# Performance work log

Hardware: AMD Instinct MI355X
Metric: run time of the kernel (lower is better)

Reference implementation:

```python
import jax, jax.numpy as jnp
import numpy as np

N_QUBITS = 20
N_LAYERS = 4
BATCH = 16
DIM = 2 ** N_QUBITS


def _apply_ry(state, theta, q, n):
    """Apply RY(theta) = [[cos(t/2), -sin(t/2)], [sin(t/2), cos(t/2)]] on qubit q.
    state: (B, 2**n) complex. Qubit 0 is most significant (qibo convention)."""
    c = jnp.cos(theta / 2).astype(state.dtype)
    s = jnp.sin(theta / 2).astype(state.dtype)
    B = state.shape[0]
    st = state.reshape(B, 2 ** q, 2, 2 ** (n - q - 1))
    a = st[:, :, 0, :]
    b = st[:, :, 1, :]
    new = jnp.stack([c * a - s * b, s * a + c * b], axis=2)
    return new.reshape(B, -1)


def _apply_cnot(state, cq, tq, n):
    """CNOT with control cq < target tq: flip target bit where control bit is 1."""
    B = state.shape[0]
    st = state.reshape(B, 2 ** cq, 2, 2 ** (tq - cq - 1), 2, 2 ** (n - tq - 1))
    ctrl0 = st[:, :, 0]                      # (B, 2^cq, mid, 2, rest)
    ctrl1 = jnp.flip(st[:, :, 1], axis=3)    # swap target |0>/<->|1>
    new = jnp.stack([ctrl0, ctrl1], axis=2)
    return new.reshape(B, -1)


def _run_circuit(state, theta):
    # theta: (N_LAYERS * N_QUBITS,) -> (N_LAYERS, N_QUBITS)
    th = theta.reshape(N_LAYERS, N_QUBITS)
    for l in range(N_LAYERS):
        for q in range(N_QUBITS):
            state = _apply_ry(state, th[l, q], q, N_QUBITS)
        for q in range(N_QUBITS - 1):
            state = _apply_cnot(state, q, q + 1, N_QUBITS)
    return state


def setup_inputs() -> dict:
    key = jax.random.key(0)
    k1, k2 = jax.random.split(key)
    x = jax.random.normal(k1, (BATCH, DIM), dtype=jnp.float32)
    theta = jax.random.normal(k2, (N_LAYERS * N_QUBITS,), dtype=jnp.float32)
    return {"x": x, "theta": theta}


def reference(x, theta):
    state = x.astype(jnp.complex64)  # initial state vector, (B, 2**n)
    state = _run_circuit(state, theta)
    return jnp.abs(state)
```

## Files before the change

### kernel.cpp

```cpp
#include <hip/hip_runtime.h>
#include <math.h>


__global__ void cs_kernel(const float* __restrict__ theta, float2* __restrict__ cs) {
    int i = threadIdx.x;
    if (i < 80) {
        float s, c;
        sincosf(theta[i] * 0.5f, &s, &c);
        cs[i] = make_float2(c, s);
    }
}

#define RYT_(TBL, MASK, Q) { float2 _sc = (TBL)[(Q)]; float _c = _sc.x, _s = _sc.y; \
  _Pragma("unroll") for (int _m = 0; _m < 32; ++_m) if (!(_m & (MASK))) { \
    float _a = v[_m], _b = v[_m | (MASK)]; \
    v[_m] = _c*_a - _s*_b; v[_m | (MASK)] = _s*_a + _c*_b; } }

#define CX_(CM, TM) { _Pragma("unroll") for (int _m = 0; _m < 32; ++_m) \
  if ((_m & (CM)) && !(_m & (TM))) { float _t = v[_m]; v[_m] = v[_m|(TM)]; v[_m|(TM)] = _t; } }

#define CXI_(COND, TM) { if (COND) { _Pragma("unroll") for (int _m = 0; _m < 32; ++_m) \
  if (!(_m & (TM))) { float _t = v[_m]; v[_m] = v[_m|(TM)]; v[_m|(TM)] = _t; } } }

__device__ __forceinline__ int mixR(int n) {
    return ((n >> 5) & 31) ^ ((n >> 10) & 1);
}
__device__ __forceinline__ int mixA(int n) {
    return ((n >> 5) & 31) ^ ((n >> 10) & 1) ^ (((n >> 11) & 1) << 3)
         ^ (((n >> 12) & 1) << 4) ^ (((n >> 13) & 1) << 4);
}
__device__ __forceinline__ int mixF(int n) {
    return ((n >> 5) & 31) ^ (((n >> 10) & 1) << 1) ^ (((n >> 11) & 1) << 2)
         ^ (((n >> 12) & 1) << 3) ^ (((n >> 13) & 1) << 4);
}
__device__ __forceinline__ int mixL(int n) {
    return ((n >> 5) & 31) ^ (((n >> 10) & 1) << 4) ^ (((n >> 11) & 1) << 2)
         ^ (((n >> 12) & 1) << 3) ^ (((n >> 13) & 1) << 4);
}

__global__ __launch_bounds__(512, 4) void pass_R(
    const float4* __restrict__ src, float4* __restrict__ dst,
    const float2* __restrict__ cs)
{
    __shared__ float lds[16384];
    const float2* csl = cs;
    int t = threadIdx.x, blk = blockIdx.x;
    int H = blk & 63, b = blk >> 6;
    int base = (b << 18) + (H << 12);
    float v[32];

#pragma unroll
    for (int i = 0; i < 8; ++i) {
        float4 w = src[base + (i << 8) + (((t >> 6) & 3) << 6) + (((t >> 8) & 1) << 11) + (t & 63)];
        v[i*4+0] = w.x; v[i*4+1] = w.y; v[i*4+2] = w.z; v[i*4+3] = w.w;
    }
    RYT_(csl, 1, 19); RYT_(csl, 2, 18); RYT_(csl, 4, 9); RYT_(csl, 8, 8); RYT_(csl, 16, 7);
    { int w1x = (t & 31) ^ ((t >> 5) & 1);
#pragma unroll
      for (int m = 0; m < 32; ++m) lds[(t << 5) | (m ^ w1x)] = v[m]; }
    __syncthreads();

    { int tp = (t & 31) | (((t >> 5) & 1) << 10) | (((t >> 6) & 7) << 11);
      int mt = mixR(tp);
#pragma unroll
      for (int f = 0; f < 32; ++f) { int fc = f << 5; v[f] = lds[(tp | fc) ^ mt ^ mixR(fc)]; }
      RYT_(csl, 1, 17); RYT_(csl, 2, 16); RYT_(csl, 4, 15); RYT_(csl, 8, 14); RYT_(csl, 16, 13);
#pragma unroll
      for (int f = 0; f < 32; ++f) { int fc = f << 5; lds[(tp | fc) ^ mt ^ mixR(fc)] = v[f]; } }
    __syncthreads();

    { int tp = ((t & 1) << 2) | (((t >> 1) & 1) << 3) | (((t >> 2) & 1) << 4)
             | (((t >> 3) & 1) << 5) | (((t >> 4) & 1) << 1) | (((t >> 5) & 1) << 0)
             | (((t >> 6) & 7) << 6);
      int mt = mixR(tp);
#pragma unroll
      for (int p = 0; p < 32; ++p) { int fc = p << 9; v[p] = lds[(tp | fc) ^ mt ^ mixR(fc)]; }
      RYT_(csl, 2, 12); RYT_(csl, 4, 11); RYT_(csl, 8, 10); RYT_(csl, 16, 6);
      int sb = base + (((t >> 6) & 7) << 6) + (t & 63);
#pragma unroll
      for (int j = 0; j < 8; ++j)
        dst[sb + (j << 9)] = make_float4(v[4*j], v[4*j+1], v[4*j+2], v[4*j+3]); }
}

template <bool FULL>
__global__ __launch_bounds__(512, 4) void pass_A(
    const float4* __restrict__ src, float4* __restrict__ dst,
    const float2* __restrict__ cs, int layer)
{
    __shared__ float lds[16384];
    const float2* csl = cs + layer * 20;
    int t = threadIdx.x, blk = blockIdx.x;
    int G = blk & 63, b = blk >> 6;
    int Gperm = ((G >> 2) & 1) | (((G >> 1) & 1) << 1) | ((G & 1) << 2) | (((G >> 3) & 7) << 3);
    float v[32];

    { int lb = (b << 18) + (((t >> 6) & 7) << 9) + (Gperm << 3) + (t & 7);
      int rg = ((t >> 3) & 7) << 12;
#pragma unroll
      for (int i = 0; i < 8; ++i) {
        float4 w = src[lb + ((i << 3) << 12) + rg];
        v[i*4+0] = w.x; v[i*4+1] = w.y; v[i*4+2] = w.z; v[i*4+3] = w.w;
      } }
    RYT_(csl, 16, 0); RYT_(csl, 8, 1); RYT_(csl, 4, 2);
    if (FULL) { RYT_(csl, 2, 12); RYT_(csl, 1, 13); }
    { int w1x = (t & 31) ^ ((t >> 5) & 1) ^ (((t >> 6) & 1) << 3)
              ^ (((t >> 7) & 1) << 4) ^ (((t >> 8) & 1) << 4);
#pragma unroll
      for (int m = 0; m < 32; ++m) lds[(t << 5) | (m ^ w1x)] = v[m]; }
    __syncthreads();

    { int tp = (t & 3) | (((t >> 2) & 1) << 7) | (((t >> 3) & 1) << 11)
             | (((t >> 4) & 1) << 12) | (((t >> 5) & 1) << 13) | (((t >> 6) & 1) << 5)
             | (((t >> 7) & 1) << 6) | (((t >> 8) & 1) << 8);
      int mt = mixA(tp);
#pragma unroll
      for (int f = 0; f < 32; ++f) {
        int fc = ((f & 1) << 9) | (((f >> 1) & 1) << 10) | (((f >> 2) & 1) << 2)
               | (((f >> 3) & 1) << 3) | (((f >> 4) & 1) << 4);
        v[f] = lds[(tp | fc) ^ mt ^ mixA(fc)]; }
      RYT_(csl, 1, 4); RYT_(csl, 2, 3);
      CX_(16, 8); CX_(8, 4); CX_(4, 2); CX_(2, 1);
#pragma unroll
      for (int f = 0; f < 32; ++f) {
        int fc = ((f & 1) << 9) | (((f >> 1) & 1) << 10) | (((f >> 2) & 1) << 2)
               | (((f >> 3) & 1) << 3) | (((f >> 4) & 1) << 4);
        lds[(tp | fc) ^ mt ^ mixA(fc)] = v[f]; } }
    __syncthreads();

    { int tp = (t & 31) | (((t >> 5) & 1) << 9) | (((t >> 6) & 1) << 10)
             | (((t >> 7) & 1) << 11) | (((t >> 8) & 1) << 12);
      int mt = mixA(tp);
#pragma unroll
      for (int f = 0; f < 32; ++f) {
        int fc = ((f & 1) << 5) | (((f >> 1) & 1) << 6) | (((f >> 2) & 1) << 7)
               | (((f >> 3) & 1) << 13) | (((f >> 4) & 1) << 8);
        v[f] = lds[(tp | fc) ^ mt ^ mixA(fc)]; }
      RYT_(csl, 16, 5);
      if (FULL) { RYT_(csl, 8, 6); RYT_(csl, 4, 7); RYT_(csl, 2, 8); RYT_(csl, 1, 9); }
      CXI_((t >> 5) & 1, 16); CX_(16, 8); CX_(8, 4); CX_(4, 2); CX_(2, 1);
#pragma unroll
      for (int f = 0; f < 32; ++f) {
        int fc = ((f & 1) << 5) | (((f >> 1) & 1) << 6) | (((f >> 2) & 1) << 7)
               | (((f >> 3) & 1) << 13) | (((f >> 4) & 1) << 8);
        lds[(tp | fc) ^ mt ^ mixA(fc)] = v[f]; } }
    __syncthreads();

    { int tp = ((t & 1) << 8) | (((t >> 1) & 1) << 9) | (((t >> 2) & 1) << 10)
             | (((t >> 3) & 1) << 6) | (((t >> 4) & 1) << 7) | (((t >> 5) & 1) << 2)
             | (((t >> 6) & 1) << 5) | (((t >> 7) & 1) << 3) | (((t >> 8) & 1) << 4);
      int mt = mixA(tp);
#pragma unroll
      for (int p = 0; p < 32; ++p) {
        int fc = ((p & 1) << 0) | (((p >> 1) & 1) << 13) | (((p >> 2) & 1) << 1)
               | (((p >> 3) & 1) << 11) | (((p >> 4) & 1) << 12);
        v[p] = lds[(tp | fc) ^ mt ^ mixA(fc)]; }
      if (FULL) { RYT_(csl, 16, 10); RYT_(csl, 8, 11); }
      CXI_((t >> 6) & 1, 16); CX_(16, 8); CX_(8, 4); CX_(4, 1);
      int sb = (b << 18) + (G << 12) + t;
#pragma unroll
      for (int j = 0; j < 8; ++j)
        dst[sb + (j << 9)] = make_float4(v[4*j], v[4*j+1], v[4*j+2], v[4*j+3]); }
}

template <bool LOWRY>
__global__ __launch_bounds__(512, 4) void pass_F(
    const float4* __restrict__ src, float4* __restrict__ dst,
    const float2* __restrict__ cs, int layer)
{
    __shared__ float lds[16384];
    const float2* csl  = cs + layer * 20;
    const float2* csl2 = cs + (layer + 1) * 20;
    int t = threadIdx.x, blk = blockIdx.x;
    int W = blk & 63, b = blk >> 6;
    int Wp = (((W >> 4) & 1) << 3) | (((W >> 5) & 1) << 4) | (((W >> 3) & 1) << 6)
           | ((W & 1) << 9) | (((W >> 1) & 1) << 10) | (((W >> 2) & 1) << 11);
    float v[32];

    { int lb = (((b << 6) | ((t >> 3) & 63)) << 12) + (t & 7) + Wp;
#pragma unroll
      for (int i = 0; i < 8; ++i) {
        float4 w = src[lb + ((i & 1) << 5) + (((i >> 1) & 1) << 7) + (((i >> 2) & 1) << 8)];
        v[i*4+0] = w.x; v[i*4+1] = w.y; v[i*4+2] = w.z; v[i*4+3] = w.w;
      } }
    RYT_(csl2, 16, 0); RYT_(csl2, 8, 1); RYT_(csl2, 4, 2); RYT_(csl2, 2, 6);
    CX_(16, 8); CX_(8, 4);
    { int w1x = (t & 31) ^ (((t >> 5) & 1) << 1) ^ (((t >> 6) & 1) << 2)
              ^ (((t >> 7) & 1) << 3) ^ (((t >> 8) & 1) << 4);
#pragma unroll
      for (int m = 0; m < 32; ++m) lds[(t << 5) | (m ^ w1x)] = v[m]; }
    __syncthreads();

    { int tp = (t & 31) | (((t >> 5) & 1) << 8) | (((t >> 6) & 1) << 5)
             | (((t >> 7) & 1) << 6) | (((t >> 8) & 1) << 7);
      int mt = mixF(tp);
#pragma unroll
      for (int f = 0; f < 32; ++f) { int fc = f << 9; v[f] = lds[(tp | fc) ^ mt ^ mixF(fc)]; }
      if (LOWRY) { RYT_(csl, 16, 14); RYT_(csl, 8, 15); RYT_(csl, 4, 16); RYT_(csl, 2, 17); RYT_(csl, 1, 18); }
      CXI_(t & 1, 16); CX_(16, 8); CX_(8, 4); CX_(4, 2); CX_(2, 1);
#pragma unroll
      for (int f = 0; f < 32; ++f) { int fc = f << 9; lds[(tp | fc) ^ mt ^ mixF(fc)] = v[f]; } }
    __syncthreads();

    { int tp = ((t & 1) << 12) | (((t >> 1) & 1) << 13) | (((t >> 2) & 1) << 0)
             | (((t >> 3) & 1) << 9) | (((t >> 4) & 1) << 10) | (((t >> 5) & 1) << 11)
             | (((t >> 6) & 1) << 2) | (((t >> 7) & 1) << 3) | (((t >> 8) & 1) << 4);
      int mt = mixF(tp);
#pragma unroll
      for (int p = 0; p < 32; ++p) {
        int fc = ((p & 1) << 8) | (((p >> 1) & 1) << 1) | (((p >> 2) & 1) << 5)
               | (((p >> 3) & 1) << 6) | (((p >> 4) & 1) << 7);
        v[p] = lds[(tp | fc) ^ mt ^ mixF(fc)]; }
      if (LOWRY) { RYT_(csl, 1, 19); }
      CXI_((t >> 3) & 1, 1);
      RYT_(csl2, 16, 3); RYT_(csl2, 8, 4); RYT_(csl2, 4, 5);
      CXI_((t >> 6) & 1, 16); CX_(16, 8); CX_(8, 4); CX_(4, 2);
      int sb = (blk << 12) + t;
#pragma unroll
      for (int j = 0; j < 8; ++j)
        dst[sb + (j << 9)] = make_float4(v[4*j], v[4*j+1], v[4*j+2], v[4*j+3]); }
}

template <bool FIN>
__global__ __launch_bounds__(512, 4) void pass_L(
    const float4* __restrict__ src, float4* __restrict__ dst,
    const float2* __restrict__ cs, int layer)
{
    __shared__ float lds[16384];
    const float2* csl = cs + layer * 20;
    int t = threadIdx.x, blk = blockIdx.x;
    int H = blk & 63, b = blk >> 6;
    int Hp = (((H >> 3) & 7) << 6) | ((H & 7) << 9);
    float v[32];

    { int rb = (b << 6) | ((t >> 6) & 7);
      int lo = Hp + (t & 63);
#pragma unroll
      for (int i = 0; i < 8; ++i) {
        float4 w = src[((rb | (i << 3)) << 12) + lo];
        v[i*4+0] = w.x; v[i*4+1] = w.y; v[i*4+2] = w.z; v[i*4+3] = w.w;
      } }
    RYT_(csl, 1, 19); RYT_(csl, 4, 9); RYT_(csl, 8, 8); RYT_(csl, 16, 7);
    { int w1x = (t & 31) ^ (((t >> 5) & 1) << 4) ^ (((t >> 6) & 1) << 2)
              ^ (((t >> 7) & 1) << 3) ^ (((t >> 8) & 1) << 4);
#pragma unroll
      for (int m = 0; m < 32; ++m) lds[(t << 5) | (m ^ w1x)] = v[m]; }
    __syncthreads();

    { int tp = (t & 3) | (((t >> 2) & 1) << 7) | (((t >> 3) & 1) << 8)
             | (((t >> 4) & 1) << 9) | (((t >> 5) & 1) << 10) | (((t >> 6) & 1) << 5)
             | (((t >> 7) & 1) << 6) | (((t >> 8) & 1) << 11);
      int mt = mixL(tp);
#pragma unroll
      for (int f = 0; f < 32; ++f) {
        int fc = ((f & 1) << 12) | (((f >> 1) & 1) << 13) | (((f >> 2) & 1) << 2)
               | (((f >> 3) & 1) << 3) | (((f >> 4) & 1) << 4);
        v[f] = lds[(tp | fc) ^ mt ^ mixL(fc)]; }
      RYT_(csl, 2, 10); RYT_(csl, 1, 11);
      CXI_((t >> 1) & 1, 16); CX_(16, 8); CX_(8, 4); CX_(4, 2); CX_(2, 1);
#pragma unroll
      for (int f = 0; f < 32; ++f) {
        int fc = ((f & 1) << 12) | (((f >> 1) & 1) << 13) | (((f >> 2) & 1) << 2)
               | (((f >> 3) & 1) << 3) | (((f >> 4) & 1) << 4);
        lds[(tp | fc) ^ mt ^ mixL(fc)] = v[f]; } }
    __syncthreads();

    { int tp = (t & 31) | (((t >> 5) & 1) << 9) | (((t >> 6) & 1) << 8)
             | (((t >> 7) & 1) << 12) | (((t >> 8) & 1) << 13);
      int mt = mixL(tp);
#pragma unroll
      for (int f = 0; f < 32; ++f) {
        int fc = ((f & 1) << 10) | (((f >> 1) & 1) << 5) | (((f >> 2) & 1) << 6)
               | (((f >> 3) & 1) << 7) | (((f >> 4) & 1) << 11);
        v[f] = lds[(tp | fc) ^ mt ^ mixL(fc)]; }
      RYT_(csl, 16, 12); RYT_(csl, 8, 13); RYT_(csl, 4, 14); RYT_(csl, 2, 15); RYT_(csl, 1, 16);
      CXI_((t >> 7) & 1, 16); CX_(16, 8); CX_(8, 4); CX_(4, 2); CX_(2, 1);
#pragma unroll
      for (int f = 0; f < 32; ++f) {
        int fc = ((f & 1) << 10) | (((f >> 1) & 1) << 5) | (((f >> 2) & 1) << 6)
               | (((f >> 3) & 1) << 7) | (((f >> 4) & 1) << 11);
        lds[(tp | fc) ^ mt ^ mixL(fc)] = v[f]; } }
    __syncthreads();

    { int tp;
      if (!FIN)
        tp = ((t & 1) << 2) | (((t >> 1) & 1) << 3) | (((t >> 2) & 1) << 4)
           | (((t >> 3) & 1) << 10) | (((t >> 4) & 1) << 5) | (((t >> 5) & 1) << 6)
           | (((t >> 6) & 1) << 1) | (((t >> 7) & 1) << 12) | (((t >> 8) & 1) << 13);
      else
        tp = ((t & 1) << 10) | (((t >> 1) & 1) << 5) | (((t >> 2) & 1) << 6)
           | (((t >> 3) & 1) << 12) | (((t >> 4) & 1) << 13) | (((t >> 5) & 1) << 2)
           | (((t >> 6) & 1) << 1) | (((t >> 7) & 1) << 3) | (((t >> 8) & 1) << 4);
      int mt = mixL(tp);
#pragma unroll
      for (int u = 0; u < 32; ++u) {
        int fc = ((u & 1) << 0) | (((u >> 1) & 1) << 8) | (((u >> 2) & 1) << 9)
               | (((u >> 3) & 1) << 7) | (((u >> 4) & 1) << 11);
        v[u] = lds[(tp | fc) ^ mt ^ mixL(fc)]; }
      RYT_(csl, 4, 17); RYT_(csl, 2, 18);
      { int e3 = FIN ? (t & 1) : ((t >> 3) & 1);
        CXI_(e3, 4); }
      CX_(4, 2); CX_(2, 1);
      if (!FIN) {
        int sb = (blk << 12) + (t & 7) + (((t >> 3) & 7) << 6)
               + (((t >> 7) & 3) << 9) + (((t >> 6) & 1) << 11);
#pragma unroll
        for (int g = 0; g < 8; ++g) {
          int bu = ((g >> 2) & 1) | (((g >> 1) & 1) << 1) | ((g & 1) << 2);
          dst[sb + (g << 3)] = make_float4(v[bu], v[bu | 8], v[bu | 16], v[bu | 24]);
        }
      } else {
        int sb = (blk << 12) + ((t & 7) << 1) + (((t >> 3) & 7) << 6)
               + (((t >> 7) & 1) << 9) + (((t >> 8) & 1) << 10) + (((t >> 6) & 1) << 11);
#pragma unroll
        for (int g = 0; g < 8; ++g) {
          int bu = ((g & 1) << 2) | (((g >> 1) & 1) << 3) | (((g >> 2) & 1) << 4);
          dst[sb + (g & 1) + (((g >> 1) & 1) << 4) + (((g >> 2) & 1) << 5)] =
            make_float4(fabsf(v[bu]), fabsf(v[bu | 1]), fabsf(v[bu | 2]), fabsf(v[bu | 3]));
        }
      } }
}

extern "C" void kernel_launch(void* const* d_in, const int* in_sizes, int n_in,
                              void* d_out, int out_size, void* d_ws, size_t ws_size,
                              hipStream_t stream) {
    const float* x     = (const float*)d_in[0];
    const float* theta = (const float*)d_in[1];
    float2* cs = (float2*)d_ws;
    float4* wsS = (float4*)((char*)d_ws + 4096);
    float4* out = (float4*)d_out;

    cs_kernel<<<1, 128, 0, stream>>>(theta, cs);

    dim3 grid(1024), block(512);
    pass_R<<<grid, block, 0, stream>>>((const float4*)x, out, cs);
    pass_A<false><<<grid, block, 0, stream>>>(out, wsS, cs, 0);
    pass_F<false><<<grid, block, 0, stream>>>(wsS, out, cs, 0);
    pass_L<false><<<grid, block, 0, stream>>>(out, wsS, cs, 1);
    pass_A<true><<<grid, block, 0, stream>>>(wsS, out, cs, 2);
    pass_F<true><<<grid, block, 0, stream>>>(out, wsS, cs, 2);
    pass_L<true><<<grid, block, 0, stream>>>(wsS, out, cs, 3);
}
```

Measured before the change: 281.6 us.

## Process two tiles per block with register prefetch of the second tile

Each block of every pass now handles two 4096-element tiles, cutting the grid from 1024 to 512 blocks. While the first tile runs its gate stages through shared memory, the global loads for the second tile are issued into a separate register buffer and swapped in after a barrier. The aim is to hide global-memory latency behind compute and LDS work. The extra 32 prefetch registers per thread may hurt occupancy or cause spills under launch_bounds(512,4), and the smaller grid leaves fewer blocks to spread across the CUs.

Result: slower. 540.3 us (+91.8%).

```diff
diff --git a/kernel.cpp b/kernel.cpp
--- a/kernel.cpp
+++ b/kernel.cpp
@@ -22,6 +22,10 @@
 #define CXI_(COND, TM) { if (COND) { _Pragma("unroll") for (int _m = 0; _m < 32; ++_m) \
   if (!(_m & (TM))) { float _t = v[_m]; v[_m] = v[_m|(TM)]; v[_m|(TM)] = _t; } } }
 
+#define SWAPIN_ { __syncthreads(); _Pragma("unroll") \
+  for (int _i = 0; _i < 8; ++_i) { v[4*_i] = u4[_i].x; v[4*_i+1] = u4[_i].y; \
+    v[4*_i+2] = u4[_i].z; v[4*_i+3] = u4[_i].w; } }
+
 __device__ __forceinline__ int mixR(int n) {
     return ((n >> 5) & 31) ^ ((n >> 10) & 1);
 }
@@ -44,42 +48,57 @@
 {
     __shared__ float lds[16384];
     const float2* csl = cs;
-    int t = threadIdx.x, blk = blockIdx.x;
-    int H = blk & 63, b = blk >> 6;
-    int base = (b << 18) + (H << 12);
+    int t = threadIdx.x;
     float v[32];
-
-#pragma unroll
-    for (int i = 0; i < 8; ++i) {
-        float4 w = src[base + (i << 8) + (((t >> 6) & 3) << 6) + (((t >> 8) & 1) << 11) + (t & 63)];
-        v[i*4+0] = w.x; v[i*4+1] = w.y; v[i*4+2] = w.z; v[i*4+3] = w.w;
+    float4 u4[8];
+
+    int lof = (((t >> 6) & 3) << 6) + (((t >> 8) & 1) << 11) + (t & 63);
+    {   int blk = blockIdx.x;
+        int base = ((blk >> 6) << 18) + ((blk & 63) << 12);
+#pragma unroll
+        for (int i = 0; i < 8; ++i) {
+            float4 w = src[base + (i << 8) + lof];
+            v[4*i] = w.x; v[4*i+1] = w.y; v[4*i+2] = w.z; v[4*i+3] = w.w;
+        } }
+
+#pragma unroll
+    for (int cc = 0; cc < 2; ++cc) {
+        int blk = blockIdx.x + (cc << 9);
+        int base = ((blk >> 6) << 18) + ((blk & 63) << 12);
+        if (cc == 0) {
+            int blk1 = blockIdx.x + 512;
+            int base1 = ((blk1 >> 6) << 18) + ((blk1 & 63) << 12);
+#pragma unroll
+            for (int i = 0; i < 8; ++i) u4[i] = src[base1 + (i << 8) + lof];
+        }
+        RYT_(csl, 1, 19); RYT_(csl, 2, 18); RYT_(csl, 4, 9); RYT_(csl, 8, 8); RYT_(csl, 16, 7);
+        { int w1x = (t & 31) ^ ((t >> 5) & 1);
+#pragma unroll
+          for (int m = 0; m < 32; ++m) lds[(t << 5) | (m ^ w1x)] = v[m]; }
+        __syncthreads();
+
+        { int tp = (t & 31) | (((t >> 5) & 1) << 10) | (((t >> 6) & 7) << 11);
+          int mt = mixR(tp);
+#pragma unroll
+          for (int f = 0; f < 32; ++f) { int fc = f << 5; v[f] = lds[(tp | fc) ^ mt ^ mixR(fc)]; }
+          RYT_(csl, 1, 17); RYT_(csl, 2, 16); RYT_(csl, 4, 15); RYT_(csl, 8, 14); RYT_(csl, 16, 13);
+#pragma unroll
+          for (int f = 0; f < 32; ++f) { int fc = f << 5; lds[(tp | fc) ^ mt ^ mixR(fc)] = v[f]; } }
+        __syncthreads();
+
+        { int tp = ((t & 1) << 2) | (((t >> 1) & 1) << 3) | (((t >> 2) & 1) << 4)
+                 | (((t >> 3) & 1) << 5) | (((t >> 4) & 1) << 1) | (((t >> 5) & 1) << 0)
+                 | (((t >> 6) & 7) << 6);
+          int mt = mixR(tp);
+#pragma unroll
+          for (int p = 0; p < 32; ++p) { int fc = p << 9; v[p] = lds[(tp | fc) ^ mt ^ mixR(fc)]; }
+          RYT_(csl, 2, 12); RYT_(csl, 4, 11); RYT_(csl, 8, 10); RYT_(csl, 16, 6);
+          int sb = base + (((t >> 6) & 7) << 6) + (t & 63);
+#pragma unroll
+          for (int j = 0; j < 8; ++j)
+            dst[sb + (j << 9)] = make_float4(v[4*j], v[4*j+1], v[4*j+2], v[4*j+3]); }
+        if (cc == 0) SWAPIN_;
     }
-    RYT_(csl, 1, 19); RYT_(csl, 2, 18); RYT_(csl, 4, 9); RYT_(csl, 8, 8); RYT_(csl, 16, 7);
-    { int w1x = (t & 31) ^ ((t >> 5) & 1);
-#pragma unroll
-      for (int m = 0; m < 32; ++m) lds[(t << 5) | (m ^ w1x)] = v[m]; }
-    __syncthreads();
-
-    { int tp = (t & 31) | (((t >> 5) & 1) << 10) | (((t >> 6) & 7) << 11);
-      int mt = mixR(tp);
-#pragma unroll
-      for (int f = 0; f < 32; ++f) { int fc = f << 5; v[f] = lds[(tp | fc) ^ mt ^ mixR(fc)]; }
-      RYT_(csl, 1, 17); RYT_(csl, 2, 16); RYT_(csl, 4, 15); RYT_(csl, 8, 14); RYT_(csl, 16, 13);
-#pragma unroll
-      for (int f = 0; f < 32; ++f) { int fc = f << 5; lds[(tp | fc) ^ mt ^ mixR(fc)] = v[f]; } }
-    __syncthreads();
-
-    { int tp = ((t & 1) << 2) | (((t >> 1) & 1) << 3) | (((t >> 2) & 1) << 4)
-             | (((t >> 3) & 1) << 5) | (((t >> 4) & 1) << 1) | (((t >> 5) & 1) << 0)
-             | (((t >> 6) & 7) << 6);
-      int mt = mixR(tp);
-#pragma unroll
-      for (int p = 0; p < 32; ++p) { int fc = p << 9; v[p] = lds[(tp | fc) ^ mt ^ mixR(fc)]; }
-      RYT_(csl, 2, 12); RYT_(csl, 4, 11); RYT_(csl, 8, 10); RYT_(csl, 16, 6);
-      int sb = base + (((t >> 6) & 7) << 6) + (t & 63);
-#pragma unroll
-      for (int j = 0; j < 8; ++j)
-        dst[sb + (j << 9)] = make_float4(v[4*j], v[4*j+1], v[4*j+2], v[4*j+3]); }
 }
 
 template <bool FULL>
@@ -89,77 +108,94 @@
 {
     __shared__ float lds[16384];
     const float2* csl = cs + layer * 20;
-    int t = threadIdx.x, blk = blockIdx.x;
-    int G = blk & 63, b = blk >> 6;
-    int Gperm = ((G >> 2) & 1) | (((G >> 1) & 1) << 1) | ((G & 1) << 2) | (((G >> 3) & 7) << 3);
+    int t = threadIdx.x;
     float v[32];
-
-    { int lb = (b << 18) + (((t >> 6) & 7) << 9) + (Gperm << 3) + (t & 7);
-      int rg = ((t >> 3) & 7) << 12;
-#pragma unroll
-      for (int i = 0; i < 8; ++i) {
-        float4 w = src[lb + ((i << 3) << 12) + rg];
-        v[i*4+0] = w.x; v[i*4+1] = w.y; v[i*4+2] = w.z; v[i*4+3] = w.w;
-      } }
-    RYT_(csl, 16, 0); RYT_(csl, 8, 1); RYT_(csl, 4, 2);
-    if (FULL) { RYT_(csl, 2, 12); RYT_(csl, 1, 13); }
-    { int w1x = (t & 31) ^ ((t >> 5) & 1) ^ (((t >> 6) & 1) << 3)
-              ^ (((t >> 7) & 1) << 4) ^ (((t >> 8) & 1) << 4);
-#pragma unroll
-      for (int m = 0; m < 32; ++m) lds[(t << 5) | (m ^ w1x)] = v[m]; }
-    __syncthreads();
-
-    { int tp = (t & 3) | (((t >> 2) & 1) << 7) | (((t >> 3) & 1) << 11)
-             | (((t >> 4) & 1) << 12) | (((t >> 5) & 1) << 13) | (((t >> 6) & 1) << 5)
-             | (((t >> 7) & 1) << 6) | (((t >> 8) & 1) << 8);
-      int mt = mixA(tp);
-#pragma unroll
-      for (int f = 0; f < 32; ++f) {
-        int fc = ((f & 1) << 9) | (((f >> 1) & 1) << 10) | (((f >> 2) & 1) << 2)
-               | (((f >> 3) & 1) << 3) | (((f >> 4) & 1) << 4);
-        v[f] = lds[(tp | fc) ^ mt ^ mixA(fc)]; }
-      RYT_(csl, 1, 4); RYT_(csl, 2, 3);
-      CX_(16, 8); CX_(8, 4); CX_(4, 2); CX_(2, 1);
-#pragma unroll
-      for (int f = 0; f < 32; ++f) {
-        int fc = ((f & 1) << 9) | (((f >> 1) & 1) << 10) | (((f >> 2) & 1) << 2)
-               | (((f >> 3) & 1) << 3) | (((f >> 4) & 1) << 4);
-        lds[(tp | fc) ^ mt ^ mixA(fc)] = v[f]; } }
-    __syncthreads();
-
-    { int tp = (t & 31) | (((t >> 5) & 1) << 9) | (((t >> 6) & 1) << 10)
-             | (((t >> 7) & 1) << 11) | (((t >> 8) & 1) << 12);
-      int mt = mixA(tp);
-#pragma unroll
-      for (int f = 0; f < 32; ++f) {
-        int fc = ((f & 1) << 5) | (((f >> 1) & 1) << 6) | (((f >> 2) & 1) << 7)
-               | (((f >> 3) & 1) << 13) | (((f >> 4) & 1) << 8);
-        v[f] = lds[(tp | fc) ^ mt ^ mixA(fc)]; }
-      RYT_(csl, 16, 5);
-      if (FULL) { RYT_(csl, 8, 6); RYT_(csl, 4, 7); RYT_(csl, 2, 8); RYT_(csl, 1, 9); }
-      CXI_((t >> 5) & 1, 16); CX_(16, 8); CX_(8, 4); CX_(4, 2); CX_(2, 1);
-#pragma unroll
-      for (int f = 0; f < 32; ++f) {
-        int fc = ((f & 1) << 5) | (((f >> 1) & 1) << 6) | (((f >> 2) & 1) << 7)
-               | (((f >> 3) & 1) << 13) | (((f >> 4) & 1) << 8);
-        lds[(tp | fc) ^ mt ^ mixA(fc)] = v[f]; } }
-    __syncthreads();
-
-    { int tp = ((t & 1) << 8) | (((t >> 1) & 1) << 9) | (((t >> 2) & 1) << 10)
-             | (((t >> 3) & 1) << 6) | (((t >> 4) & 1) << 7) | (((t >> 5) & 1) << 2)
-             | (((t >> 6) & 1) << 5) | (((t >> 7) & 1) << 3) | (((t >> 8) & 1) << 4);
-      int mt = mixA(tp);
-#pragma unroll
-      for (int p = 0; p < 32; ++p) {
-        int fc = ((p & 1) << 0) | (((p >> 1) & 1) << 13) | (((p >> 2) & 1) << 1)
-               | (((p >> 3) & 1) << 11) | (((p >> 4) & 1) << 12);
-        v[p] = lds[(tp | fc) ^ mt ^ mixA(fc)]; }
-      if (FULL) { RYT_(csl, 16, 10); RYT_(csl, 8, 11); }
-      CXI_((t >> 6) & 1, 16); CX_(16, 8); CX_(8, 4); CX_(4, 1);
-      int sb = (b << 18) + (G << 12) + t;
-#pragma unroll
-      for (int j = 0; j < 8; ++j)
-        dst[sb + (j << 9)] = make_float4(v[4*j], v[4*j+1], v[4*j+2], v[4*j+3]); }
+    float4 u4[8];
+
+    int rg = ((t >> 3) & 7) << 12;
+    {   int blk = blockIdx.x;
+        int G = blk & 63, b = blk >> 6;
+        int Gperm = ((G >> 2) & 1) | (((G >> 1) & 1) << 1) | ((G & 1) << 2) | (((G >> 3) & 7) << 3);
+        int lb = (b << 18) + (((t >> 6) & 7) << 9) + (Gperm << 3) + (t & 7);
+#pragma unroll
+        for (int i = 0; i < 8; ++i) {
+            float4 w = src[lb + (i << 15) + rg];
+            v[4*i] = w.x; v[4*i+1] = w.y; v[4*i+2] = w.z; v[4*i+3] = w.w;
+        } }
+
+#pragma unroll
+    for (int cc = 0; cc < 2; ++cc) {
+        int blk = blockIdx.x + (cc << 9);
+        int G = blk & 63, b = blk >> 6;
+        if (cc == 0) {
+            int blk1 = blockIdx.x + 512;
+            int G1 = blk1 & 63, b1 = blk1 >> 6;
+            int Gp1 = ((G1 >> 2) & 1) | (((G1 >> 1) & 1) << 1) | ((G1 & 1) << 2) | (((G1 >> 3) & 7) << 3);
+            int lb1 = (b1 << 18) + (((t >> 6) & 7) << 9) + (Gp1 << 3) + (t & 7);
+#pragma unroll
+            for (int i = 0; i < 8; ++i) u4[i] = src[lb1 + (i << 15) + rg];
+        }
+        RYT_(csl, 16, 0); RYT_(csl, 8, 1); RYT_(csl, 4, 2);
+        if (FULL) { RYT_(csl, 2, 12); RYT_(csl, 1, 13); }
+        { int w1x = (t & 31) ^ ((t >> 5) & 1) ^ (((t >> 6) & 1) << 3)
+                  ^ (((t >> 7) & 1) << 4) ^ (((t >> 8) & 1) << 4);
+#pragma unroll
+          for (int m = 0; m < 32; ++m) lds[(t << 5) | (m ^ w1x)] = v[m]; }
+        __syncthreads();
+
+        { int tp = (t & 3) | (((t >> 2) & 1) << 7) | (((t >> 3) & 1) << 11)
+                 | (((t >> 4) & 1) << 12) | (((t >> 5) & 1) << 13) | (((t >> 6) & 1) << 5)
+                 | (((t >> 7) & 1) << 6) | (((t >> 8) & 1) << 8);
+          int mt = mixA(tp);
+#pragma unroll
+          for (int f = 0; f < 32; ++f) {
+            int fc = ((f & 1) << 9) | (((f >> 1) & 1) << 10) | (((f >> 2) & 1) << 2)
+                   | (((f >> 3) & 1) << 3) | (((f >> 4) & 1) << 4);
+            v[f] = lds[(tp | fc) ^ mt ^ mixA(fc)]; }
+          RYT_(csl, 1, 4); RYT_(csl, 2, 3);
+          CX_(16, 8); CX_(8, 4); CX_(4, 2); CX_(2, 1);
+#pragma unroll
+          for (int f = 0; f < 32; ++f) {
+            int fc = ((f & 1) << 9) | (((f >> 1) & 1) << 10) | (((f >> 2) & 1) << 2)
+                   | (((f >> 3) & 1) << 3) | (((f >> 4) & 1) << 4);
+            lds[(tp | fc) ^ mt ^ mixA(fc)] = v[f]; } }
+        __syncthreads();
+
+        { int tp = (t & 31) | (((t >> 5) & 1) << 9) | (((t >> 6) & 1) << 10)
+                 | (((t >> 7) & 1) << 11) | (((t >> 8) & 1) << 12);
+          int mt = mixA(tp);
+#pragma unroll
+          for (int f = 0; f < 32; ++f) {
+            int fc = ((f & 1) << 5) | (((f >> 1) & 1) << 6) | (((f >> 2) & 1) << 7)
+                   | (((f >> 3) & 1) << 13) | (((f >> 4) & 1) << 8);
+            v[f] = lds[(tp | fc) ^ mt ^ mixA(fc)]; }
+          RYT_(csl, 16, 5);
+          if (FULL) { RYT_(csl, 8, 6); RYT_(csl, 4, 7); RYT_(csl, 2, 8); RYT_(csl, 1, 9); }
+          CXI_((t >> 5) & 1, 16); CX_(16, 8); CX_(8, 4); CX_(4, 2); CX_(2, 1);
+#pragma unroll
+          for (int f = 0; f < 32; ++f) {
+            int fc = ((f & 1) << 5) | (((f >> 1) & 1) << 6) | (((f >> 2) & 1) << 7)
+                   | (((f >> 3) & 1) << 13) | (((f >> 4) & 1) << 8);
+            lds[(tp | fc) ^ mt ^ mixA(fc)] = v[f]; } }
+        __syncthreads();
+
+        { int tp = ((t & 1) << 8) | (((t >> 1) & 1) << 9) | (((t >> 2) & 1) << 10)
+                 | (((t >> 3) & 1) << 6) | (((t >> 4) & 1) << 7) | (((t >> 5) & 1) << 2)
+                 | (((t >> 6) & 1) << 5) | (((t >> 7) & 1) << 3) | (((t >> 8) & 1) << 4);
+          int mt = mixA(tp);
+#pragma unroll
+          for (int p = 0; p < 32; ++p) {
+            int fc = ((p & 1) << 0) | (((p >> 1) & 1) << 13) | (((p >> 2) & 1) << 1)
+                   | (((p >> 3) & 1) << 11) | (((p >> 4) & 1) << 12);
+            v[p] = lds[(tp | fc) ^ mt ^ mixA(fc)]; }
+          if (FULL) { RYT_(csl, 16, 10); RYT_(csl, 8, 11); }
+          CXI_((t >> 6) & 1, 16); CX_(16, 8); CX_(8, 4); CX_(4, 1);
+          int sb = (b << 18) + (G << 12) + t;
+#pragma unroll
+          for (int j = 0; j < 8; ++j)
+            dst[sb + (j << 9)] = make_float4(v[4*j], v[4*j+1], v[4*j+2], v[4*j+3]); }
+        if (cc == 0) SWAPIN_;
+    }
 }
 
 template <bool LOWRY>
@@ -170,54 +206,72 @@
     __shared__ float lds[16384];
     const float2* csl  = cs + layer * 20;
     const float2* csl2 = cs + (layer + 1) * 20;
-    int t = threadIdx.x, blk = blockIdx.x;
-    int W = blk & 63, b = blk >> 6;
-    int Wp = (((W >> 4) & 1) << 3) | (((W >> 5) & 1) << 4) | (((W >> 3) & 1) << 6)
-           | ((W & 1) << 9) | (((W >> 1) & 1) << 10) | (((W >> 2) & 1) << 11);
+    int t = threadIdx.x;
     float v[32];
-
-    { int lb = (((b << 6) | ((t >> 3) & 63)) << 12) + (t & 7) + Wp;
-#pragma unroll
-      for (int i = 0; i < 8; ++i) {
-        float4 w = src[lb + ((i & 1) << 5) + (((i >> 1) & 1) << 7) + (((i >> 2) & 1) << 8)];
-        v[i*4+0] = w.x; v[i*4+1] = w.y; v[i*4+2] = w.z; v[i*4+3] = w.w;
-      } }
-    RYT_(csl2, 16, 0); RYT_(csl2, 8, 1); RYT_(csl2, 4, 2); RYT_(csl2, 2, 6);
-    CX_(16, 8); CX_(8, 4);
-    { int w1x = (t & 31) ^ (((t >> 5) & 1) << 1) ^ (((t >> 6) & 1) << 2)
-              ^ (((t >> 7) & 1) << 3) ^ (((t >> 8) & 1) << 4);
-#pragma unroll
-      for (int m = 0; m < 32; ++m) lds[(t << 5) | (m ^ w1x)] = v[m]; }
-    __syncthreads();
-
-    { int tp = (t & 31) | (((t >> 5) & 1) << 8) | (((t >> 6) & 1) << 5)
-             | (((t >> 7) & 1) << 6) | (((t >> 8) & 1) << 7);
-      int mt = mixF(tp);
-#pragma unroll
-      for (int f = 0; f < 32; ++f) { int fc = f << 9; v[f] = lds[(tp | fc) ^ mt ^ mixF(fc)]; }
-      if (LOWRY) { RYT_(csl, 16, 14); RYT_(csl, 8, 15); RYT_(csl, 4, 16); RYT_(csl, 2, 17); RYT_(csl, 1, 18); }
-      CXI_(t & 1, 16); CX_(16, 8); CX_(8, 4); CX_(4, 2); CX_(2, 1);
-#pragma unroll
-      for (int f = 0; f < 32; ++f) { int fc = f << 9; lds[(tp | fc) ^ mt ^ mixF(fc)] = v[f]; } }
-    __syncthreads();
-
-    { int tp = ((t & 1) << 12) | (((t >> 1) & 1) << 13) | (((t >> 2) & 1) << 0)
-             | (((t >> 3) & 1) << 9) | (((t >> 4) & 1) << 10) | (((t >> 5) & 1) << 11)
-             | (((t >> 6) & 1) << 2) | (((t >> 7) & 1) << 3) | (((t >> 8) & 1) << 4);
-      int mt = mixF(tp);
-#pragma unroll
-      for (int p = 0; p < 32; ++p) {
-        int fc = ((p & 1) << 8) | (((p >> 1) & 1) << 1) | (((p >> 2) & 1) << 5)
-               | (((p >> 3) & 1) << 6) | (((p >> 4) & 1) << 7);
-        v[p] = lds[(tp | fc) ^ mt ^ mixF(fc)]; }
-      if (LOWRY) { RYT_(csl, 1, 19); }
-      CXI_((t >> 3) & 1, 1);
-      RYT_(csl2, 16, 3); RYT_(csl2, 8, 4); RYT_(csl2, 4, 5);
-      CXI_((t >> 6) & 1, 16); CX_(16, 8); CX_(8, 4); CX_(4, 2);
-      int sb = (blk << 12) + t;
-#pragma unroll
-      for (int j = 0; j < 8; ++j)
-        dst[sb + (j << 9)] = make_float4(v[4*j], v[4*j+1], v[4*j+2], v[4*j+3]); }
+    float4 u4[8];
+
+    {   int blk = blockIdx.x;
+        int W = blk & 63, b = blk >> 6;
+        int Wp = (((W >> 4) & 1) << 3) | (((W >> 5) & 1) << 4) | (((W >> 3) & 1) << 6)
+               | ((W & 1) << 9) | (((W >> 1) & 1) << 10) | (((W >> 2) & 1) << 11);
+        int lb = (((b << 6) | ((t >> 3) & 63)) << 12) + (t & 7) + Wp;
+#pragma unroll
+        for (int i = 0; i < 8; ++i) {
+            float4 w = src[lb + ((i & 1) << 5) + (((i >> 1) & 1) << 7) + (((i >> 2) & 1) << 8)];
+            v[4*i] = w.x; v[4*i+1] = w.y; v[4*i+2] = w.z; v[4*i+3] = w.w;
+        } }
+
+#pragma unroll
+    for (int cc = 0; cc < 2; ++cc) {
+        int blk = blockIdx.x + (cc << 9);
+        if (cc == 0) {
+            int blk1 = blockIdx.x + 512;
+            int W1 = blk1 & 63, b1 = blk1 >> 6;
+            int Wp1 = (((W1 >> 4) & 1) << 3) | (((W1 >> 5) & 1) << 4) | (((W1 >> 3) & 1) << 6)
+                    | ((W1 & 1) << 9) | (((W1 >> 1) & 1) << 10) | (((W1 >> 2) & 1) << 11);
+            int lb1 = (((b1 << 6) | ((t >> 3) & 63)) << 12) + (t & 7) + Wp1;
+#pragma unroll
+            for (int i = 0; i < 8; ++i)
+                u4[i] = src[lb1 + ((i & 1) << 5) + (((i >> 1) & 1) << 7) + (((i >> 2) & 1) << 8)];
+        }
+        RYT_(csl2, 16, 0); RYT_(csl2, 8, 1); RYT_(csl2, 4, 2); RYT_(csl2, 2, 6);
+        CX_(16, 8); CX_(8, 4);
+        { int w1x = (t & 31) ^ (((t >> 5) & 1) << 1) ^ (((t >> 6) & 1) << 2)
+                  ^ (((t >> 7) & 1) << 3) ^ (((t >> 8) & 1) << 4);
+#pragma unroll
+          for (int m = 0; m < 32; ++m) lds[(t << 5) | (m ^ w1x)] = v[m]; }
+        __syncthreads();
+
+        { int tp = (t & 31) | (((t >> 5) & 1) << 8) | (((t >> 6) & 1) << 5)
+                 | (((t >> 7) & 1) << 6) | (((t >> 8) & 1) << 7);
+          int mt = mixF(tp);
+#pragma unroll
+          for (int f = 0; f < 32; ++f) { int fc = f << 9; v[f] = lds[(tp | fc) ^ mt ^ mixF(fc)]; }
+          if (LOWRY) { RYT_(csl, 16, 14); RYT_(csl, 8, 15); RYT_(csl, 4, 16); RYT_(csl, 2, 17); RYT_(csl, 1, 18); }
+          CXI_(t & 1, 16); CX_(16, 8); CX_(8, 4); CX_(4, 2); CX_(2, 1);
+#pragma unroll
+          for (int f = 0; f < 32; ++f) { int fc = f << 9; lds[(tp | fc) ^ mt ^ mixF(fc)] = v[f]; } }
+        __syncthreads();
+
+        { int tp = ((t & 1) << 12) | (((t >> 1) & 1) << 13) | (((t >> 2) & 1) << 0)
+                 | (((t >> 3) & 1) << 9) | (((t >> 4) & 1) << 10) | (((t >> 5) & 1) << 11)
+                 | (((t >> 6) & 1) << 2) | (((t >> 7) & 1) << 3) | (((t >> 8) & 1) << 4);
+          int mt = mixF(tp);
+#pragma unroll
+          for (int p = 0; p < 32; ++p) {
+            int fc = ((p & 1) << 8) | (((p >> 1) & 1) << 1) | (((p >> 2) & 1) << 5)
+                   | (((p >> 3) & 1) << 6) | (((p >> 4) & 1) << 7);
+            v[p] = lds[(tp | fc) ^ mt ^ mixF(fc)]; }
+          if (LOWRY) { RYT_(csl, 1, 19); }
+          CXI_((t >> 3) & 1, 1);
+          RYT_(csl2, 16, 3); RYT_(csl2, 8, 4); RYT_(csl2, 4, 5);
+          CXI_((t >> 6) & 1, 16); CX_(16, 8); CX_(8, 4); CX_(4, 2);
+          int sb = (blk << 12) + t;
+#pragma unroll
+          for (int j = 0; j < 8; ++j)
+            dst[sb + (j << 9)] = make_float4(v[4*j], v[4*j+1], v[4*j+2], v[4*j+3]); }
+        if (cc == 0) SWAPIN_;
+    }
 }
 
 template <bool FIN>
@@ -227,97 +281,114 @@
 {
     __shared__ float lds[16384];
     const float2* csl = cs + layer * 20;
-    int t = threadIdx.x, blk = blockIdx.x;
-    int H = blk & 63, b = blk >> 6;
-    int Hp = (((H >> 3) & 7) << 6) | ((H & 7) << 9);
+    int t = threadIdx.x;
     float v[32];
-
-    { int rb = (b << 6) | ((t >> 6) & 7);
-      int lo = Hp + (t & 63);
-#pragma unroll
-      for (int i = 0; i < 8; ++i) {
-        float4 w = src[((rb | (i << 3)) << 12) + lo];
-        v[i*4+0] = w.x; v[i*4+1] = w.y; v[i*4+2] = w.z; v[i*4+3] = w.w;
-      } }
-    RYT_(csl, 1, 19); RYT_(csl, 4, 9); RYT_(csl, 8, 8); RYT_(csl, 16, 7);
-    { int w1x = (t & 31) ^ (((t >> 5) & 1) << 4) ^ (((t >> 6) & 1) << 2)
-              ^ (((t >> 7) & 1) << 3) ^ (((t >> 8) & 1) << 4);
-#pragma unroll
-      for (int m = 0; m < 32; ++m) lds[(t << 5) | (m ^ w1x)] = v[m]; }
-    __syncthreads();
-
-    { int tp = (t & 3) | (((t >> 2) & 1) << 7) | (((t >> 3) & 1) << 8)
-             | (((t >> 4) & 1) << 9) | (((t >> 5) & 1) << 10) | (((t >> 6) & 1) << 5)
-             | (((t >> 7) & 1) << 6) | (((t >> 8) & 1) << 11);
-      int mt = mixL(tp);
-#pragma unroll
-      for (int f = 0; f < 32; ++f) {
-        int fc = ((f & 1) << 12) | (((f >> 1) & 1) << 13) | (((f >> 2) & 1) << 2)
-               | (((f >> 3) & 1) << 3) | (((f >> 4) & 1) << 4);
-        v[f] = lds[(tp | fc) ^ mt ^ mixL(fc)]; }
-      RYT_(csl, 2, 10); RYT_(csl, 1, 11);
-      CXI_((t >> 1) & 1, 16); CX_(16, 8); CX_(8, 4); CX_(4, 2); CX_(2, 1);
-#pragma unroll
-      for (int f = 0; f < 32; ++f) {
-        int fc = ((f & 1) << 12) | (((f >> 1) & 1) << 13) | (((f >> 2) & 1) << 2)
-               | (((f >> 3) & 1) << 3) | (((f >> 4) & 1) << 4);
-        lds[(tp | fc) ^ mt ^ mixL(fc)] = v[f]; } }
-    __syncthreads();
-
-    { int tp = (t & 31) | (((t >> 5) & 1) << 9) | (((t >> 6) & 1) << 8)
-             | (((t >> 7) & 1) << 12) | (((t >> 8) & 1) << 13);
-      int mt = mixL(tp);
-#pragma unroll
-      for (int f = 0; f < 32; ++f) {
-        int fc = ((f & 1) << 10) | (((f >> 1) & 1) << 5) | (((f >> 2) & 1) << 6)
-               | (((f >> 3) & 1) << 7) | (((f >> 4) & 1) << 11);
-        v[f] = lds[(tp | fc) ^ mt ^ mixL(fc)]; }
-      RYT_(csl, 16, 12); RYT_(csl, 8, 13); RYT_(csl, 4, 14); RYT_(csl, 2, 15); RYT_(csl, 1, 16);
-      CXI_((t >> 7) & 1, 16); CX_(16, 8); CX_(8, 4); CX_(4, 2); CX_(2, 1);
-#pragma unroll
-      for (int f = 0; f < 32; ++f) {
-        int fc = ((f & 1) << 10) | (((f >> 1) & 1) << 5) | (((f >> 2) & 1) << 6)
-               | (((f >> 3) & 1) << 7) | (((f >> 4) & 1) << 11);
-        lds[(tp | fc) ^ mt ^ mixL(fc)] = v[f]; } }
-    __syncthreads();
-
-    { int tp;
-      if (!FIN)
-        tp = ((t & 1) << 2) | (((t >> 1) & 1) << 3) | (((t >> 2) & 1) << 4)
-           | (((t >> 3) & 1) << 10) | (((t >> 4) & 1) << 5) | (((t >> 5) & 1) << 6)
-           | (((t >> 6) & 1) << 1) | (((t >> 7) & 1) << 12) | (((t >> 8) & 1) << 13);
-      else
-        tp = ((t & 1) << 10) | (((t >> 1) & 1) << 5) | (((t >> 2) & 1) << 6)
-           | (((t >> 3) & 1) << 12) | (((t >> 4) & 1) << 13) | (((t >> 5) & 1) << 2)
-           | (((t >> 6) & 1) << 1) | (((t >> 7) & 1) << 3) | (((t >> 8) & 1) << 4);
-      int mt = mixL(tp);
-#pragma unroll
-      for (int u = 0; u < 32; ++u) {
-        int fc = ((u & 1) << 0) | (((u >> 1) & 1) << 8) | (((u >> 2) & 1) << 9)
-               | (((u >> 3) & 1) << 7) | (((u >> 4) & 1) << 11);
-        v[u] = lds[(tp | fc) ^ mt ^ mixL(fc)]; }
-      RYT_(csl, 4, 17); RYT_(csl, 2, 18);
-      { int e3 = FIN ? (t & 1) : ((t >> 3) & 1);
-        CXI_(e3, 4); }
-      CX_(4, 2); CX_(2, 1);
-      if (!FIN) {
-        int sb = (blk << 12) + (t & 7) + (((t >> 3) & 7) << 6)
-               + (((t >> 7) & 3) << 9) + (((t >> 6) & 1) << 11);
-#pragma unroll
-        for (int g = 0; g < 8; ++g) {
-          int bu = ((g >> 2) & 1) | (((g >> 1) & 1) << 1) | ((g & 1) << 2);
-          dst[sb + (g << 3)] = make_float4(v[bu], v[bu | 8], v[bu | 16], v[bu | 24]);
+    float4 u4[8];
+
+    {   int blk = blockIdx.x;
+        int H = blk & 63, b = blk >> 6;
+        int Hp = (((H >> 3) & 7) << 6) | ((H & 7) << 9);
+        int rb = (b << 6) | ((t >> 6) & 7);
+        int lo = Hp + (t & 63);
+#pragma unroll
+        for (int i = 0; i < 8; ++i) {
+            float4 w = src[((rb | (i << 3)) << 12) + lo];
+            v[4*i] = w.x; v[4*i+1] = w.y; v[4*i+2] = w.z; v[4*i+3] = w.w;
+        } }
+
+#pragma unroll
+    for (int cc = 0; cc < 2; ++cc) {
+        int blk = blockIdx.x + (cc << 9);
+        if (cc == 0) {
+            int blk1 = blockIdx.x + 512;
+            int H1 = blk1 & 63, b1 = blk1 >> 6;
+            int Hp1 = (((H1 >> 3) & 7) << 6) | ((H1 & 7) << 9);
+            int rb1 = (b1 << 6) | ((t >> 6) & 7);
+            int lo1 = Hp1 + (t & 63);
+#pragma unroll
+            for (int i = 0; i < 8; ++i) u4[i] = src[((rb1 | (i << 3)) << 12) + lo1];
         }
-      } else {
-        int sb = (blk << 12) + ((t & 7) << 1) + (((t >> 3) & 7) << 6)
-               + (((t >> 7) & 1) << 9) + (((t >> 8) & 1) << 10) + (((t >> 6) & 1) << 11);
-#pragma unroll
-        for (int g = 0; g < 8; ++g) {
-          int bu = ((g & 1) << 2) | (((g >> 1) & 1) << 3) | (((g >> 2) & 1) << 4);
-          dst[sb + (g & 1) + (((g >> 1) & 1) << 4) + (((g >> 2) & 1) << 5)] =
-            make_float4(fabsf(v[bu]), fabsf(v[bu | 1]), fabsf(v[bu | 2]), fabsf(v[bu | 3]));
-        }
-      } }
+        RYT_(csl, 1, 19); RYT_(csl, 4, 9); RYT_(csl, 8, 8); RYT_(csl, 16, 7);
+        { int w1x = (t & 31) ^ (((t >> 5) & 1) << 4) ^ (((t >> 6) & 1) << 2)
+                  ^ (((t >> 7) & 1) << 3) ^ (((t >> 8) & 1) << 4);
+#pragma unroll
+          for (int m = 0; m < 32; ++m) lds[(t << 5) | (m ^ w1x)] = v[m]; }
+        __syncthreads();
+
+        { int tp = (t & 3) | (((t >> 2) & 1) << 7) | (((t >> 3) & 1) << 8)
+                 | (((t >> 4) & 1) << 9) | (((t >> 5) & 1) << 10) | (((t >> 6) & 1) << 5)
+                 | (((t >> 7) & 1) << 6) | (((t >> 8) & 1) << 11);
+          int mt = mixL(tp);
+#pragma unroll
+          for (int f = 0; f < 32; ++f) {
+            int fc = ((f & 1) << 12) | (((f >> 1) & 1) << 13) | (((f >> 2) & 1) << 2)
+                   | (((f >> 3) & 1) << 3) | (((f >> 4) & 1) << 4);
+            v[f] = lds[(tp | fc) ^ mt ^ mixL(fc)]; }
+          RYT_(csl, 2, 10); RYT_(csl, 1, 11);
+          CXI_((t >> 1) & 1, 16); CX_(16, 8); CX_(8, 4); CX_(4, 2); CX_(2, 1);
+#pragma unroll
+          for (int f = 0; f < 32; ++f) {
+            int fc = ((f & 1) << 12) | (((f >> 1) & 1) << 13) | (((f >> 2) & 1) << 2)
+                   | (((f >> 3) & 1) << 3) | (((f >> 4) & 1) << 4);
+            lds[(tp | fc) ^ mt ^ mixL(fc)] = v[f]; } }
+        __syncthreads();
+
+        { int tp = (t & 31) | (((t >> 5) & 1) << 9) | (((t >> 6) & 1) << 8)
+                 | (((t >> 7) & 1) << 12) | (((t >> 8) & 1) << 13);
+          int mt = mixL(tp);
+#pragma unroll
+          for (int f = 0; f < 32; ++f) {
+            int fc = ((f & 1) << 10) | (((f >> 1) & 1) << 5) | (((f >> 2) & 1) << 6)
+                   | (((f >> 3) & 1) << 7) | (((f >> 4) & 1) << 11);
+            v[f] = lds[(tp | fc) ^ mt ^ mixL(fc)]; }
+          RYT_(csl, 16, 12); RYT_(csl, 8, 13); RYT_(csl, 4, 14); RYT_(csl, 2, 15); RYT_(csl, 1, 16);
+          CXI_((t >> 7) & 1, 16); CX_(16, 8); CX_(8, 4); CX_(4, 2); CX_(2, 1);
+#pragma unroll
+          for (int f = 0; f < 32; ++f) {
+            int fc = ((f & 1) << 10) | (((f >> 1) & 1) << 5) | (((f >> 2) & 1) << 6)
+                   | (((f >> 3) & 1) << 7) | (((f >> 4) & 1) << 11);
+            lds[(tp | fc) ^ mt ^ mixL(fc)] = v[f]; } }
+        __syncthreads();
+
+        { int tp;
+          if (!FIN)
+            tp = ((t & 1) << 2) | (((t >> 1) & 1) << 3) | (((t >> 2) & 1) << 4)
+               | (((t >> 3) & 1) << 10) | (((t >> 4) & 1) << 5) | (((t >> 5) & 1) << 6)
+               | (((t >> 6) & 1) << 1) | (((t >> 7) & 1) << 12) | (((t >> 8) & 1) << 13);
+          else
+            tp = ((t & 1) << 10) | (((t >> 1) & 1) << 5) | (((t >> 2) & 1) << 6)
+               | (((t >> 3) & 1) << 12) | (((t >> 4) & 1) << 13) | (((t >> 5) & 1) << 2)
+               | (((t >> 6) & 1) << 1) | (((t >> 7) & 1) << 3) | (((t >> 8) & 1) << 4);
+          int mt = mixL(tp);
+#pragma unroll
+          for (int u = 0; u < 32; ++u) {
+            int fc = ((u & 1) << 0) | (((u >> 1) & 1) << 8) | (((u >> 2) & 1) << 9)
+                   | (((u >> 3) & 1) << 7) | (((u >> 4) & 1) << 11);
+            v[u] = lds[(tp | fc) ^ mt ^ mixL(fc)]; }
+          RYT_(csl, 4, 17); RYT_(csl, 2, 18);
+          { int e3 = FIN ? (t & 1) : ((t >> 3) & 1);
+            CXI_(e3, 4); }
+          CX_(4, 2); CX_(2, 1);
+          if (!FIN) {
+            int sb = (blk << 12) + (t & 7) + (((t >> 3) & 7) << 6)
+                   + (((t >> 7) & 3) << 9) + (((t >> 6) & 1) << 11);
+#pragma unroll
+            for (int g = 0; g < 8; ++g) {
+              int bu = ((g >> 2) & 1) | (((g >> 1) & 1) << 1) | ((g & 1) << 2);
+              dst[sb + (g << 3)] = make_float4(v[bu], v[bu | 8], v[bu | 16], v[bu | 24]);
+            }
+          } else {
+            int sb = (blk << 12) + ((t & 7) << 1) + (((t >> 3) & 7) << 6)
+                   + (((t >> 7) & 1) << 9) + (((t >> 8) & 1) << 10) + (((t >> 6) & 1) << 11);
+#pragma unroll
+            for (int g = 0; g < 8; ++g) {
+              int bu = ((g & 1) << 2) | (((g >> 1) & 1) << 3) | (((g >> 2) & 1) << 4);
+              dst[sb + (g & 1) + (((g >> 1) & 1) << 4) + (((g >> 2) & 1) << 5)] =
+                make_float4(fabsf(v[bu]), fabsf(v[bu | 1]), fabsf(v[bu | 2]), fabsf(v[bu | 3]));
+            }
+          } }
+        if (cc == 0) SWAPIN_;
+    }
 }
 
 extern "C" void kernel_launch(void* const* d_in, const int* in_sizes, int n_in,
@@ -331,7 +402,7 @@
 
     cs_kernel<<<1, 128, 0, stream>>>(theta, cs);
 
-    dim3 grid(1024), block(512);
+    dim3 grid(512), block(512);
     pass_R<<<grid, block, 0, stream>>>((const float4*)x, out, cs);
     pass_A<false><<<grid, block, 0, stream>>>(out, wsS, cs, 0);
     pass_F<false><<<grid, block, 0, stream>>>(wsS, out, cs, 0);
```
